# Optimization experiments

Measured on AMD Instinct MI355X. Metric: run time of the kernel, lower is better.

## Reference

```python
import jax, jax.numpy as jnp
import numpy as np

NEG_SLOPE = 0.01  # torch F.leaky_relu default

def _lrelu(x):
    return jax.nn.leaky_relu(x, NEG_SLOPE)

def setup_inputs() -> dict:
    key = jax.random.key(0)
    ks = jax.random.split(key, 24)
    B, N, E = 512, 20000, 640000
    n_enc_1, n_enc_2, n_z = 512, 256, 64
    n_dec_2, n_dec_1, hidden = 256, 512, 256
    p = lambda k, shp, fan: jax.random.normal(k, shp, jnp.float32) * (1.0 / np.sqrt(fan))
    return {
        "data": jax.random.normal(ks[0], (B, N), jnp.float32),
        "noise": jax.random.normal(ks[1], (B, N), jnp.float32),
        "edge_index": jax.random.randint(ks[2], (2, E), 0, N, jnp.int32),
        "w_gcn": jax.random.normal(ks[3], (), jnp.float32),
        "b_gcn": jax.random.normal(ks[4], (), jnp.float32) * 0.1,
        "enc1_w": p(ks[5], (N, n_enc_1), N), "enc1_b": p(ks[6], (n_enc_1,), N),
        "enc2_w": p(ks[7], (n_enc_1, n_enc_2), n_enc_1), "enc2_b": p(ks[8], (n_enc_2,), n_enc_1),
        "enc3_w": p(ks[9], (n_enc_2, n_z), n_enc_2), "enc3_b": p(ks[10], (n_z,), n_enc_2),
        "dec1_w": p(ks[11], (n_z, n_dec_2), n_z), "dec1_b": p(ks[12], (n_dec_2,), n_z),
        "dec2_w": p(ks[13], (n_dec_2, n_dec_1), n_dec_2), "dec2_b": p(ks[14], (n_dec_1,), n_dec_2),
        "dec3_w": p(ks[15], (n_dec_1, N), n_dec_1), "dec3_b": p(ks[16], (N,), n_dec_1),
        "disc1_w": p(ks[17], (n_z, hidden), n_z), "disc1_b": p(ks[18], (hidden,), n_z),
        "disc2_w": p(ks[19], (hidden, hidden), hidden), "disc2_b": p(ks[20], (hidden,), hidden),
        "disc3_w": p(ks[21], (hidden, 1), hidden), "disc3_b": p(ks[22], (1,), hidden),
    }

def _gcn_batched(x, edge_index, w_gcn, b_gcn):
    # x: [B, N] -> GCNConv(1,1, improved=True) applied per row, vectorized.
    B, N = x.shape
    src, dst = edge_index[0], edge_index[1]
    loop = jnp.arange(N, dtype=src.dtype)
    src_a = jnp.concatenate([src, loop])
    dst_a = jnp.concatenate([dst, loop])
    # improved=True: self-loop edge weight 2.0
    ew = jnp.concatenate([jnp.ones(src.shape[0], x.dtype), jnp.full((N,), 2.0, x.dtype)])
    deg = jax.ops.segment_sum(ew, dst_a, num_segments=N)
    dinv = jnp.where(deg > 0, jax.lax.rsqrt(deg), 0.0)
    norm = dinv[src_a] * ew * dinv[dst_a]  # [E+N]
    xl = x * w_gcn                         # lin (1x1 weight, no bias)
    msgs = xl[:, src_a] * norm[None, :]    # [B, E+N]
    agg = jnp.zeros_like(x).at[:, dst_a].add(msgs)
    return agg + b_gcn

def reference(data, noise, edge_index, w_gcn, b_gcn,
              enc1_w, enc1_b, enc2_w, enc2_b, enc3_w, enc3_b,
              dec1_w, dec1_b, dec2_w, dec2_b, dec3_w, dec3_b,
              disc1_w, disc1_b, disc2_w, disc2_b, disc3_w, disc3_b):
    x = data + noise * 0.1
    gcn_out = _lrelu(_gcn_batched(x, edge_index, w_gcn, b_gcn))  # [B, N]
    h1 = _lrelu(gcn_out @ enc1_w + enc1_b)
    h2 = _lrelu(h1 @ enc2_w + enc2_b)
    z = _lrelu(h2 @ enc3_w + enc3_b)
    d1 = _lrelu(z @ dec1_w + dec1_b)
    d2 = _lrelu(d1 @ dec2_w + dec2_b)
    dec_h3 = _lrelu(d2 @ dec3_w + dec3_b)
    g1 = _lrelu(z @ disc1_w + disc1_b)
    g2 = _lrelu(g1 @ disc2_w + disc2_b)
    d = jax.nn.sigmoid(g2 @ disc3_w + disc3_b)
    return (dec_h3, z, d)
```

## Files before the change

### kernel.cpp

```cpp
#include <hip/hip_runtime.h>
#include <hip/hip_bf16.h>


#define LRELU(v) ((v) > 0.f ? (v) : 0.01f * (v))

static constexpr int Bb = 512;
static constexpr int Nn = 20000;
static constexpr int Ee = 640000;
static constexpr int KPAD = 20480;
static constexpr int NPD = 20096;
static constexpr int RSU = 36;
static constexpr int RSW = 18;

typedef __attribute__((ext_vector_type(8))) short short8;
typedef __attribute__((ext_vector_type(4))) short short4v;
typedef __attribute__((ext_vector_type(4))) float f32x4;

__device__ __forceinline__ ushort f2bf(float f) {
  uint u = __builtin_bit_cast(uint, f);
  u = u + 0x7FFFu + ((u >> 16) & 1u);
  return (ushort)(u >> 16);
}
__device__ __forceinline__ float bfLo(uint u) {
  return __builtin_bit_cast(float, u << 16);
}
__device__ __forceinline__ float bfHi(uint u) {
  return __builtin_bit_cast(float, u & 0xffff0000u);
}

__global__ void transpose_xs_k(const float* __restrict__ a, const float* __restrict__ nz,
                               const float* __restrict__ dinv, ushort* __restrict__ xs) {
  __shared__ ushort tile[64][65];
  int c0 = blockIdx.x * 64;
  int p = blockIdx.y;
  int chunk = p >> 1;
  int sub = (p & 1) * 64;
  int rbase = p * 64;
  for (int i = threadIdx.x; i < 64 * 64; i += 256) {
    int rr = i >> 6, cc = i & 63;
    int r = rbase + rr, c = c0 + cc;
    ushort v = 0;
    if (c < Nn) {
      size_t idx = (size_t)r * Nn + c;
      v = f2bf(dinv[c] * (a[idx] + 0.1f * nz[idx]));
    }
    tile[rr][cc] = v;
  }
  __syncthreads();
  for (int i = threadIdx.x; i < 64 * 64; i += 256) {
    int cc = i >> 6, rr = i & 63;
    int c = c0 + cc;
    if (c < Nn) xs[(size_t)chunk * Nn * 128 + (size_t)c * 128 + sub + rr] = tile[rr][cc];
  }
}

__global__ void hist_check_k(const int* __restrict__ src, const int* __restrict__ dst, int E,
                             int* __restrict__ cnt, int* __restrict__ flag) {
  int i = blockIdx.x * 256 + threadIdx.x;
  if (i < E) {
    int s = src[i], d = dst[i];
    if ((unsigned)s >= (unsigned)Nn || (unsigned)d >= (unsigned)Nn) {
      atomicExch(flag, 1);
    } else {
      atomicAdd(&cnt[d], 1);
    }
  }
}

__global__ void offs_k(const int* __restrict__ cnt, int* __restrict__ offs,
                       int* __restrict__ cursor, float* __restrict__ dinv,
                       int* __restrict__ bump) {
  int i = blockIdx.x * 256 + threadIdx.x;
  int l = threadIdx.x & 63;
  int v = (i < Nn) ? cnt[i] : 0;
  int x = v;
#pragma unroll
  for (int d = 1; d < 64; d <<= 1) {
    int t = __shfl_up(x, d);
    if (l >= d) x += t;
  }
  int total = __shfl(x, 63);
  int base = 0;
  if (l == 0) base = atomicAdd(bump, total);
  base = __shfl(base, 0);
  int excl = base + x - v;
  if (i < Nn) {
    offs[i] = excl;
    cursor[i] = excl;
    dinv[i] = rsqrtf(2.0f + (float)v);
  }
}

__global__ void scatter_k(const int* __restrict__ src, const int* __restrict__ dst, int E,
                          int* __restrict__ cursor, uint* __restrict__ eOff) {
  int i = blockIdx.x * 256 + threadIdx.x;
  if (i < E) {
    int s = src[i], d = dst[i];
    if ((unsigned)s >= (unsigned)Nn || (unsigned)d >= (unsigned)Nn) return;
    int p = atomicAdd(&cursor[d], 1);
    eOff[p] = (uint)s * 256u;
  }
}

__global__ __launch_bounds__(256) void spmm_chunk_k(
    const ushort* __restrict__ xs, const uint* __restrict__ eOff, const int* __restrict__ offs,
    const int* __restrict__ cnt, const float* __restrict__ dinv, const float* __restrict__ wg,
    const float* __restrict__ bg, ushort* __restrict__ gcnT) {
  __shared__ uint sIdx[4][64];
  int bid = blockIdx.x;
  int chunk = bid & 3;
  int ngrp = bid >> 2;
  int wv = threadIdx.x >> 6, l = threadIdx.x & 63;
  int n = ngrp * 4 + wv;
  int o = offs[n], c = cnt[n];
  const char* base = (const char*)(xs + (size_t)chunk * Nn * 128) + l * 4;
  const uint* ep = eOff + o;
  uint su = *(const uint*)(base + (size_t)n * 256);
  float a00 = 2.0f * bfLo(su), a01 = 2.0f * bfHi(su);
  float a10 = 0.f, a11 = 0.f;

  for (int bi = 0; bi < c; bi += 64) {
    int rem = c - bi;
    if (rem > 64) rem = 64;
    sIdx[wv][l] = (l < rem) ? ep[bi + l] : 0u;
    int i = 0;
    for (; i + 8 <= rem; i += 8) {
      uint u[8];
#pragma unroll
      for (int j = 0; j < 8; ++j) u[j] = *(const uint*)(base + sIdx[wv][i + j]);
#pragma unroll
      for (int j = 0; j < 8; j += 2) {
        a00 += bfLo(u[j]);
        a01 += bfHi(u[j]);
        a10 += bfLo(u[j + 1]);
        a11 += bfHi(u[j + 1]);
      }
    }
    for (; i < rem; ++i) {
      uint u = *(const uint*)(base + sIdx[wv][i]);
      a00 += bfLo(u);
      a01 += bfHi(u);
    }
  }

  float wdn = wg[0] * dinv[n], bb = bg[0];
  float v0 = wdn * (a00 + a10) + bb;
  float v1 = wdn * (a01 + a11) + bb;
  v0 = LRELU(v0);
  v1 = LRELU(v1);
  uint pk = (uint)f2bf(v0) | ((uint)f2bf(v1) << 16);
  *(uint*)&gcnT[(size_t)chunk * KPAD * 128 + (size_t)n * 128 + 2 * l] = pk;
}

__global__ __launch_bounds__(256) void mfma_gemm4(const ushort* __restrict__ AT,
                                                  const float* __restrict__ B, int KB,
                                                  int iters, float* __restrict__ C) {
  __shared__ ushort As[128 * RSU];
  __shared__ ushort Bs[128 * RSU];
  int n0 = blockIdx.x * 128, m0 = blockIdx.y * 128;
  int k0 = blockIdx.z * iters * 32;
  int tid = threadIdx.x;
  int kp = tid >> 4;
  int cpr = tid & 15;
  int c8 = cpr * 8;
  int l = tid & 63, w = tid >> 6;
  int wr = w >> 1, wc = w & 1;
  int lrow = l & 15, lkg = l >> 4;
  const ushort* Ap = AT + (size_t)(m0 >> 7) * ((size_t)KPAD * 128);
  int bcol = n0 + c8;
  int kps = kp ^ (((cpr >> 1) & 3) << 2);
  f32x4 acc[4][4] = {};

  uint4 pa0, pa1;
  float4 pb00, pb01, pb10, pb11;

#define GLOAD(KG)                                                              \
  {                                                                            \
    int kq = (KG) + 2 * kp;                                                    \
    pa0 = *(const uint4*)&Ap[(size_t)kq * 128 + c8];                           \
    pa1 = *(const uint4*)&Ap[(size_t)(kq + 1) * 128 + c8];                     \
    pb00 = pb01 = pb10 = pb11 = float4{0.f, 0.f, 0.f, 0.f};                    \
    if (kq < KB) {                                                             \
      const float4* bp = (const float4*)(B + (size_t)kq * 512 + bcol);         \
      pb00 = bp[0];                                                            \
      pb01 = bp[1];                                                            \
    }                                                                          \
    if (kq + 1 < KB) {                                                         \
      const float4* bp = (const float4*)(B + (size_t)(kq + 1) * 512 + bcol);   \
      pb10 = bp[0];                                                            \
      pb11 = bp[1];                                                            \
    }                                                                          \
  }

  GLOAD(k0);

  for (int kt = 0; kt < iters; ++kt) {
    uint wa[8], wb[8];
    wa[0] = (pa0.x & 0xffffu) | (pa1.x << 16);
    wa[1] = (pa0.x >> 16) | (pa1.x & 0xffff0000u);
    wa[2] = (pa0.y & 0xffffu) | (pa1.y << 16);
    wa[3] = (pa0.y >> 16) | (pa1.y & 0xffff0000u);
    wa[4] = (pa0.z & 0xffffu) | (pa1.z << 16);
    wa[5] = (pa0.z >> 16) | (pa1.z & 0xffff0000u);
    wa[6] = (pa0.w & 0xffffu) | (pa1.w << 16);
    wa[7] = (pa0.w >> 16) | (pa1.w & 0xffff0000u);
    wb[0] = (uint)f2bf(pb00.x) | ((uint)f2bf(pb10.x) << 16);
    wb[1] = (uint)f2bf(pb00.y) | ((uint)f2bf(pb10.y) << 16);
    wb[2] = (uint)f2bf(pb00.z) | ((uint)f2bf(pb10.z) << 16);
    wb[3] = (uint)f2bf(pb00.w) | ((uint)f2bf(pb10.w) << 16);
    wb[4] = (uint)f2bf(pb01.x) | ((uint)f2bf(pb11.x) << 16);
    wb[5] = (uint)f2bf(pb01.y) | ((uint)f2bf(pb11.y) << 16);
    wb[6] = (uint)f2bf(pb01.z) | ((uint)f2bf(pb11.z) << 16);
    wb[7] = (uint)f2bf(pb01.w) | ((uint)f2bf(pb11.w) << 16);
    __syncthreads();
    {
      uint* aw = (uint*)As;
      uint* bw = (uint*)Bs;
#pragma unroll
      for (int j = 0; j < 8; ++j) {
        aw[(c8 + j) * RSW + kps] = wa[j];
        bw[(c8 + j) * RSW + kps] = wb[j];
      }
    }
    __syncthreads();
    if (kt + 1 < iters) GLOAD(k0 + (kt + 1) * 32);
    short8 a[4], b[4];
#pragma unroll
    for (int mi = 0; mi < 4; ++mi) {
      int m = wr * 64 + mi * 16 + lrow;
      int lk2 = lkg ^ ((wr * 4 + mi) & 3);
      const short4v* p = (const short4v*)&As[m * RSU + lk2 * 8];
      a[mi] = __builtin_shufflevector(p[0], p[1], 0, 1, 2, 3, 4, 5, 6, 7);
    }
#pragma unroll
    for (int nj = 0; nj < 4; ++nj) {
      int n = wc * 64 + nj * 16 + lrow;
      int lk2 = lkg ^ ((wc * 4 + nj) & 3);
      const short4v* p = (const short4v*)&Bs[n * RSU + lk2 * 8];
      b[nj] = __builtin_shufflevector(p[0], p[1], 0, 1, 2, 3, 4, 5, 6, 7);
    }
#pragma unroll
    for (int mi = 0; mi < 4; ++mi)
#pragma unroll
      for (int nj = 0; nj < 4; ++nj)
        acc[mi][nj] = __builtin_amdgcn_mfma_f32_16x16x32_bf16(a[mi], b[nj], acc[mi][nj], 0, 0, 0);
  }
#undef GLOAD

#pragma unroll
  for (int mi = 0; mi < 4; ++mi)
#pragma unroll
    for (int nj = 0; nj < 4; ++nj)
#pragma unroll
      for (int r = 0; r < 4; ++r) {
        int row = m0 + wr * 64 + mi * 16 + lkg * 4 + r;
        int col = n0 + wc * 64 + nj * 16 + lrow;
        atomicAdd(&C[(size_t)row * 512 + col], acc[mi][nj][r]);
      }
}

__global__ void conv_wf_k(const float* __restrict__ W, ushort* __restrict__ wf) {
  int n = blockIdx.x * 256 + threadIdx.x;
  int kb = blockIdx.y;
  if (n >= NPD) return;
  ushort v[8];
#pragma unroll
  for (int j = 0; j < 8; ++j)
    v[j] = (n < Nn) ? f2bf(W[(size_t)(8 * kb + j) * Nn + n]) : (ushort)0;
  uint4 pk;
  pk.x = (uint)v[0] | ((uint)v[1] << 16);
  pk.y = (uint)v[2] | ((uint)v[3] << 16);
  pk.z = (uint)v[4] | ((uint)v[5] << 16);
  pk.w = (uint)v[6] | ((uint)v[7] << 16);
  *(uint4*)&wf[((size_t)kb * NPD + n) * 8] = pk;
}

__global__ __launch_bounds__(256) void fmg_dec3_k(const ushort* __restrict__ d2f,
                                                  const ushort* __restrict__ wf,
                                                  const float* __restrict__ bias,
                                                  float* __restrict__ C) {
  int n0 = blockIdx.x * 128, m0 = blockIdx.y * 128;
  int l = threadIdx.x & 63, w = threadIdx.x >> 6;
  int wr = w >> 1, wc = w & 1;
  int lrow = l & 15, lkg = l >> 4;
  f32x4 acc[4][4] = {};

#pragma unroll 4
  for (int ks = 0; ks < 16; ++ks) {
    int kb = ks * 4 + lkg;
    short8 a[4], b[4];
#pragma unroll
    for (int mi = 0; mi < 4; ++mi) {
      int m = m0 + wr * 64 + mi * 16 + lrow;
      a[mi] = *(const short8*)&d2f[((size_t)kb * 512 + m) * 8];
    }
#pragma unroll
    for (int nj = 0; nj < 4; ++nj) {
      int n = n0 + wc * 64 + nj * 16 + lrow;
      b[nj] = *(const short8*)&wf[((size_t)kb * NPD + n) * 8];
    }
#pragma unroll
    for (int mi = 0; mi < 4; ++mi)
#pragma unroll
      for (int nj = 0; nj < 4; ++nj)
        acc[mi][nj] = __builtin_amdgcn_mfma_f32_16x16x32_bf16(a[mi], b[nj], acc[mi][nj], 0, 0, 0);
  }

#pragma unroll
  for (int mi = 0; mi < 4; ++mi)
#pragma unroll
    for (int nj = 0; nj < 4; ++nj)
#pragma unroll
      for (int r = 0; r < 4; ++r) {
        int row = m0 + wr * 64 + mi * 16 + lkg * 4 + r;
        int col = n0 + wc * 64 + nj * 16 + lrow;
        if (col < Nn) {
          float v = acc[mi][nj][r] + bias[col];
          C[(size_t)row * Nn + col] = LRELU(v);
        }
      }
}

__global__ __launch_bounds__(256) void tail2_k(
    const float* __restrict__ h1, const float* __restrict__ c1, const float* __restrict__ W2,
    const float* __restrict__ c2, const float* __restrict__ W3, const float* __restrict__ c3,
    const float* __restrict__ Wd1, const float* __restrict__ cd1, const float* __restrict__ Wd2,
    const float* __restrict__ cd2, const float* __restrict__ Wg1, const float* __restrict__ cg1,
    const float* __restrict__ Wg2, const float* __restrict__ cg2, const float* __restrict__ Wg3,
    const float* __restrict__ cg3, float* __restrict__ out_z, float* __restrict__ out_d,
    ushort* __restrict__ d2f) {
  __shared__ float s_h1[512];
  __shared__ float s_h2[256];
  __shared__ float s_z[64];
  __shared__ float s_d1[256];
  __shared__ float s_g1[256];
  __shared__ float s_g2[256];
  __shared__ float s_part[4][256];
  __shared__ float s_red[4];
  int rl = blockIdx.x;
  int t = threadIdx.x;
  int w = t >> 6, l = t & 63;

  {
    float r0 = h1[(size_t)rl * 512 + t] + c1[t];
    float r1 = h1[(size_t)rl * 512 + t + 256] + c1[t + 256];
    s_h1[t] = LRELU(r0);
    s_h1[t + 256] = LRELU(r1);
  }
  __syncthreads();

  {
    int c4 = l * 4;
    float a0 = 0.f, a1 = 0.f, a2 = 0.f, a3 = 0.f;
#pragma unroll 8
    for (int k = w * 128; k < w * 128 + 128; ++k) {
      float4 wv = *(const float4*)&W2[(size_t)k * 256 + c4];
      float x = s_h1[k];
      a0 += x * wv.x; a1 += x * wv.y; a2 += x * wv.z; a3 += x * wv.w;
    }
    float4 pv = {a0, a1, a2, a3};
    *(float4*)&s_part[w][c4] = pv;
  }
  __syncthreads();
  s_h2[t] = LRELU(s_part[0][t] + s_part[1][t] + s_part[2][t] + s_part[3][t] + c2[t]);
  __syncthreads();

  {
    int c = t >> 2, p = t & 3;
    float a = 0.f;
#pragma unroll 8
    for (int k = p * 64; k < p * 64 + 64; ++k) a += s_h2[k] * W3[(size_t)k * 64 + c];
    s_part[p][c] = a;
  }
  __syncthreads();
  if (t < 64) {
    float v = s_part[0][t] + s_part[1][t] + s_part[2][t] + s_part[3][t] + c3[t];
    v = LRELU(v);
    s_z[t] = v;
    out_z[(size_t)rl * 64 + t] = v;
  }
  __syncthreads();

  {
    float a = 0.f;
#pragma unroll
    for (int k = 0; k < 64; ++k) a += s_z[k] * Wd1[(size_t)k * 256 + t];
    s_d1[t] = LRELU(a + cd1[t]);
  }
  {
    float a = 0.f;
#pragma unroll
    for (int k = 0; k < 64; ++k) a += s_z[k] * Wg1[(size_t)k * 256 + t];
    s_g1[t] = LRELU(a + cg1[t]);
  }
  __syncthreads();

  {
    int g = t & 127, p = t >> 7;
    int c4 = g * 4;
    float a0 = 0.f, a1 = 0.f, a2 = 0.f, a3 = 0.f;
#pragma unroll 8
    for (int k = p * 128; k < p * 128 + 128; ++k) {
      float4 wv = *(const float4*)&Wd2[(size_t)k * 512 + c4];
      float x = s_d1[k];
      a0 += x * wv.x; a1 += x * wv.y; a2 += x * wv.z; a3 += x * wv.w;
    }
    float* sp = &s_part[0][0];
    float4 pv = {a0, a1, a2, a3};
    *(float4*)&sp[p * 512 + c4] = pv;
  }
  __syncthreads();
  {
    const float* sp = &s_part[0][0];
#pragma unroll
    for (int cc = 0; cc < 2; ++cc) {
      int c = t + cc * 256;
      float v = sp[c] + sp[512 + c] + cd2[c];
      v = LRELU(v);
      d2f[((size_t)(c >> 3) * 512 + rl) * 8 + (c & 7)] = f2bf(v);
    }
  }
  __syncthreads();

  {
    int c4 = l * 4;
    float a0 = 0.f, a1 = 0.f, a2 = 0.f, a3 = 0.f;
#pragma unroll 8
    for (int k = w * 64; k < w * 64 + 64; ++k) {
      float4 wv = *(const float4*)&Wg2[(size_t)k * 256 + c4];
      float x = s_g1[k];
      a0 += x * wv.x; a1 += x * wv.y; a2 += x * wv.z; a3 += x * wv.w;
    }
    float4 pv = {a0, a1, a2, a3};
    *(float4*)&s_part[w][c4] = pv;
  }
  __syncthreads();
  s_g2[t] = LRELU(s_part[0][t] + s_part[1][t] + s_part[2][t] + s_part[3][t] + cg2[t]);
  __syncthreads();

  {
    float p = s_g2[t] * Wg3[t];
#pragma unroll
    for (int o = 32; o > 0; o >>= 1) p += __shfl_down(p, o);
    if ((t & 63) == 0) s_red[t >> 6] = p;
    __syncthreads();
    if (t == 0) {
      float s = s_red[0] + s_red[1] + s_red[2] + s_red[3] + cg3[0];
      out_d[rl] = 1.f / (1.f + __expf(-s));
    }
  }
}

__global__ void sentinel_k(float* out, float val) { out[0] = val; }
__global__ void flag_sentinel_k(float* out, const int* flag) {
  if (*flag != 0) out[0] = 70000.0f;
}

extern "C" void kernel_launch(void* const* d_in, const int* in_sizes, int n_in,
                              void* d_out, int out_size, void* d_ws, size_t ws_size,
                              hipStream_t stream) {
  const float* data = (const float*)d_in[0];
  const float* noise = (const float*)d_in[1];
  const int* edge = (const int*)d_in[2];
  const int* esrc_in = edge;
  const int* edst_in = edge + Ee;
  const float* w_gcn = (const float*)d_in[3];
  const float* b_gcn = (const float*)d_in[4];
  const float* enc1_w = (const float*)d_in[5];
  const float* enc1_b = (const float*)d_in[6];
  const float* enc2_w = (const float*)d_in[7];
  const float* enc2_b = (const float*)d_in[8];
  const float* enc3_w = (const float*)d_in[9];
  const float* enc3_b = (const float*)d_in[10];
  const float* dec1_w = (const float*)d_in[11];
  const float* dec1_b = (const float*)d_in[12];
  const float* dec2_w = (const float*)d_in[13];
  const float* dec2_b = (const float*)d_in[14];
  const float* dec3_w = (const float*)d_in[15];
  const float* dec3_b = (const float*)d_in[16];
  const float* disc1_w = (const float*)d_in[17];
  const float* disc1_b = (const float*)d_in[18];
  const float* disc2_w = (const float*)d_in[19];
  const float* disc2_b = (const float*)d_in[20];
  const float* disc3_w = (const float*)d_in[21];
  const float* disc3_b = (const float*)d_in[22];

  char* w = (char*)d_ws;
  size_t o = 0;
  auto alloc = [&](size_t bytes) {
    size_t r = o;
    o = (o + bytes + 15) & ~(size_t)15;
    return r;
  };
  size_t r1 = alloc((size_t)64 * NPD * 8 * 2);
  ushort* xs = (ushort*)(w + r1);
  ushort* wf = (ushort*)(w + r1);
  ushort* gcnT = (ushort*)(w + alloc((size_t)4 * KPAD * 128 * 2));
  float* h1 = (float*)(w + alloc(512 * 512 * 4));
  ushort* d2f = (ushort*)(w + alloc((size_t)64 * 512 * 8 * 2));
  float* dinv = (float*)(w + alloc(Nn * 4));
  int* cnt = (int*)(w + alloc(Nn * 4));
  int* offs = (int*)(w + alloc(Nn * 4));
  int* cursor = (int*)(w + alloc(Nn * 4));
  uint* eOff = (uint*)(w + alloc(Ee * 4));
  int* flag = (int*)(w + alloc(16));

  float* outp = (float*)d_out;
  float* out_dec = outp;
  float* out_z = outp + (size_t)Bb * Nn;
  float* out_d = out_z + (size_t)Bb * 64;

  static const int expect_sizes[23] = {
      10240000, 10240000, 1280000, 1, 1,
      10240000, 512, 131072, 256, 16384, 64,
      16384, 256, 131072, 512, 10240000, 20000,
      16384, 256, 65536, 256, 256, 1};
  float host_sentinel = 0.f;
  if (n_in != 23) host_sentinel = 50000.f;
  else if (out_size != 10273280) host_sentinel = 80000.f;
  else if (ws_size < 46100000u) host_sentinel = 60000.f;
  else {
    for (int i = 0; i < 23; ++i)
      if (in_sizes[i] != expect_sizes[i]) { host_sentinel = 100000.f + 1000.f * i; break; }
  }

  hipMemsetAsync(cnt, 0, Nn * sizeof(int), stream);
  hipMemsetAsync(flag, 0, 2 * sizeof(int), stream);
  hist_check_k<<<(Ee + 255) / 256, 256, 0, stream>>>(esrc_in, edst_in, Ee, cnt, flag);
  offs_k<<<(Nn + 255) / 256, 256, 0, stream>>>(cnt, offs, cursor, dinv, flag + 1);
  scatter_k<<<(Ee + 255) / 256, 256, 0, stream>>>(esrc_in, edst_in, Ee, cursor, eOff);
  for (int c = 0; c < 4; ++c)
    hipMemsetAsync(gcnT + ((size_t)c * KPAD + Nn) * 128, 0, (size_t)(KPAD - Nn) * 128 * 2,
                   stream);

  {
    dim3 g((Nn + 63) / 64, 8);
    transpose_xs_k<<<g, 256, 0, stream>>>(data, noise, dinv, xs);
  }
  spmm_chunk_k<<<(Nn / 4) * 4, 256, 0, stream>>>(xs, eOff, offs, cnt, dinv, w_gcn, b_gcn, gcnT);
  hipMemsetAsync(h1, 0, 512 * 512 * 4, stream);
  {
    dim3 g(512 / 128, 512 / 128, 32);
    mfma_gemm4<<<g, 256, 0, stream>>>(gcnT, enc1_w, Nn, 20, h1);
  }
  tail2_k<<<Bb, 256, 0, stream>>>(h1, enc1_b, enc2_w, enc2_b, enc3_w, enc3_b, dec1_w, dec1_b,
                                  dec2_w, dec2_b, disc1_w, disc1_b, disc2_w, disc2_b, disc3_w,
                                  disc3_b, out_z, out_d, d2f);
  {
    dim3 g((NPD + 255) / 256, 64);
    conv_wf_k<<<g, 256, 0, stream>>>(dec3_w, wf);
  }
  {
    dim3 g(NPD / 128, 512 / 128);
    fmg_dec3_k<<<g, 256, 0, stream>>>(d2f, wf, dec3_b, out_dec);
  }

  flag_sentinel_k<<<1, 1, 0, stream>>>(out_dec, flag);
  if (host_sentinel != 0.f) sentinel_k<<<1, 1, 0, stream>>>(out_dec, host_sentinel);
}
```

Before: 288.2 us.

## Emit GCN output in MFMA fragment layout and pre-convert enc1 weights for LDS-free GEMM

```diff
diff --git a/kernel.cpp b/kernel.cpp
--- a/kernel.cpp
+++ b/kernel.cpp
@@ -7,13 +7,10 @@
 static constexpr int Bb = 512;
 static constexpr int Nn = 20000;
 static constexpr int Ee = 640000;
-static constexpr int KPAD = 20480;
+static constexpr int KBn = 2500;
 static constexpr int NPD = 20096;
-static constexpr int RSU = 36;
-static constexpr int RSW = 18;
 
 typedef __attribute__((ext_vector_type(8))) short short8;
-typedef __attribute__((ext_vector_type(4))) short short4v;
 typedef __attribute__((ext_vector_type(4))) float f32x4;
 
 __device__ __forceinline__ ushort f2bf(float f) {
@@ -102,142 +99,104 @@
   }
 }
 
-__global__ __launch_bounds__(256) void spmm_chunk_k(
+__global__ __launch_bounds__(256) void spmm_fm_k(
     const ushort* __restrict__ xs, const uint* __restrict__ eOff, const int* __restrict__ offs,
     const int* __restrict__ cnt, const float* __restrict__ dinv, const float* __restrict__ wg,
-    const float* __restrict__ bg, ushort* __restrict__ gcnT) {
+    const float* __restrict__ bg, ushort* __restrict__ gfm) {
   __shared__ uint sIdx[4][64];
+  __shared__ ushort sOut[128][8];
   int bid = blockIdx.x;
   int chunk = bid & 3;
-  int ngrp = bid >> 2;
+  int grp = bid >> 2;
   int wv = threadIdx.x >> 6, l = threadIdx.x & 63;
-  int n = ngrp * 4 + wv;
-  int o = offs[n], c = cnt[n];
   const char* base = (const char*)(xs + (size_t)chunk * Nn * 128) + l * 4;
-  const uint* ep = eOff + o;
-  uint su = *(const uint*)(base + (size_t)n * 256);
-  float a00 = 2.0f * bfLo(su), a01 = 2.0f * bfHi(su);
-  float a10 = 0.f, a11 = 0.f;
-
-  for (int bi = 0; bi < c; bi += 64) {
-    int rem = c - bi;
-    if (rem > 64) rem = 64;
-    sIdx[wv][l] = (l < rem) ? ep[bi + l] : 0u;
-    int i = 0;
-    for (; i + 8 <= rem; i += 8) {
-      uint u[8];
-#pragma unroll
-      for (int j = 0; j < 8; ++j) u[j] = *(const uint*)(base + sIdx[wv][i + j]);
-#pragma unroll
-      for (int j = 0; j < 8; j += 2) {
-        a00 += bfLo(u[j]);
-        a01 += bfHi(u[j]);
-        a10 += bfLo(u[j + 1]);
-        a11 += bfHi(u[j + 1]);
+  float wgv = wg[0], bb = bg[0];
+
+#pragma unroll
+  for (int sub = 0; sub < 2; ++sub) {
+    int n = grp * 8 + wv * 2 + sub;
+    int o = offs[n], c = cnt[n];
+    const uint* ep = eOff + o;
+    uint su = *(const uint*)(base + (size_t)n * 256);
+    float a00 = 2.0f * bfLo(su), a01 = 2.0f * bfHi(su);
+    float a10 = 0.f, a11 = 0.f;
+
+    for (int bi = 0; bi < c; bi += 64) {
+      int rem = c - bi;
+      if (rem > 64) rem = 64;
+      sIdx[wv][l] = (l < rem) ? ep[bi + l] : 0u;
+      int i = 0;
+      for (; i + 8 <= rem; i += 8) {
+        uint u[8];
+#pragma unroll
+        for (int j = 0; j < 8; ++j) u[j] = *(const uint*)(base + sIdx[wv][i + j]);
+#pragma unroll
+        for (int j = 0; j < 8; j += 2) {
+          a00 += bfLo(u[j]);
+          a01 += bfHi(u[j]);
+          a10 += bfLo(u[j + 1]);
+          a11 += bfHi(u[j + 1]);
+        }
       }
-    }
-    for (; i < rem; ++i) {
-      uint u = *(const uint*)(base + sIdx[wv][i]);
-      a00 += bfLo(u);
-      a01 += bfHi(u);
-    }
-  }
-
-  float wdn = wg[0] * dinv[n], bb = bg[0];
-  float v0 = wdn * (a00 + a10) + bb;
-  float v1 = wdn * (a01 + a11) + bb;
-  v0 = LRELU(v0);
-  v1 = LRELU(v1);
-  uint pk = (uint)f2bf(v0) | ((uint)f2bf(v1) << 16);
-  *(uint*)&gcnT[(size_t)chunk * KPAD * 128 + (size_t)n * 128 + 2 * l] = pk;
-}
-
-__global__ __launch_bounds__(256) void mfma_gemm4(const ushort* __restrict__ AT,
-                                                  const float* __restrict__ B, int KB,
-                                                  int iters, float* __restrict__ C) {
-  __shared__ ushort As[128 * RSU];
-  __shared__ ushort Bs[128 * RSU];
+      for (; i < rem; ++i) {
+        uint u = *(const uint*)(base + sIdx[wv][i]);
+        a00 += bfLo(u);
+        a01 += bfHi(u);
+      }
+    }
+
+    float wdn = wgv * dinv[n];
+    float v0 = wdn * (a00 + a10) + bb;
+    float v1 = wdn * (a01 + a11) + bb;
+    v0 = LRELU(v0);
+    v1 = LRELU(v1);
+    int j = wv * 2 + sub;
+    sOut[2 * l][j] = f2bf(v0);
+    sOut[2 * l + 1][j] = f2bf(v1);
+  }
+  __syncthreads();
+  int row = threadIdx.x >> 1, half = threadIdx.x & 1;
+  uint2 v = *(const uint2*)&sOut[row][half * 4];
+  int m = chunk * 128 + row;
+  *(uint2*)&gfm[((size_t)grp * 512 + m) * 8 + half * 4] = v;
+}
+
+__global__ void conv_we_k(const float* __restrict__ W, ushort* __restrict__ wef) {
+  int n = blockIdx.x * 256 + threadIdx.x;
+  int kb = blockIdx.y;
+  ushort v[8];
+#pragma unroll
+  for (int j = 0; j < 8; ++j) v[j] = f2bf(W[(size_t)(8 * kb + j) * 512 + n]);
+  uint4 pk;
+  pk.x = (uint)v[0] | ((uint)v[1] << 16);
+  pk.y = (uint)v[2] | ((uint)v[3] << 16);
+  pk.z = (uint)v[4] | ((uint)v[5] << 16);
+  pk.w = (uint)v[6] | ((uint)v[7] << 16);
+  *(uint4*)&wef[((size_t)kb * 512 + n) * 8] = pk;
+}
+
+__global__ __launch_bounds__(256) void fmg_enc1_k(const ushort* __restrict__ gfm,
+                                                  const ushort* __restrict__ wef,
+                                                  float* __restrict__ C) {
   int n0 = blockIdx.x * 128, m0 = blockIdx.y * 128;
-  int k0 = blockIdx.z * iters * 32;
-  int tid = threadIdx.x;
-  int kp = tid >> 4;
-  int cpr = tid & 15;
-  int c8 = cpr * 8;
-  int l = tid & 63, w = tid >> 6;
+  int l = threadIdx.x & 63, w = threadIdx.x >> 6;
   int wr = w >> 1, wc = w & 1;
   int lrow = l & 15, lkg = l >> 4;
-  const ushort* Ap = AT + (size_t)(m0 >> 7) * ((size_t)KPAD * 128);
-  int bcol = n0 + c8;
-  int kps = kp ^ (((cpr >> 1) & 3) << 2);
   f32x4 acc[4][4] = {};
-
-  uint4 pa0, pa1;
-  float4 pb00, pb01, pb10, pb11;
-
-#define GLOAD(KG)                                                              \
-  {                                                                            \
-    int kq = (KG) + 2 * kp;                                                    \
-    pa0 = *(const uint4*)&Ap[(size_t)kq * 128 + c8];                           \
-    pa1 = *(const uint4*)&Ap[(size_t)(kq + 1) * 128 + c8];                     \
-    pb00 = pb01 = pb10 = pb11 = float4{0.f, 0.f, 0.f, 0.f};                    \
-    if (kq < KB) {                                                             \
-      const float4* bp = (const float4*)(B + (size_t)kq * 512 + bcol);         \
-      pb00 = bp[0];                                                            \
-      pb01 = bp[1];                                                            \
-    }                                                                          \
-    if (kq + 1 < KB) {                                                         \
-      const float4* bp = (const float4*)(B + (size_t)(kq + 1) * 512 + bcol);   \
-      pb10 = bp[0];                                                            \
-      pb11 = bp[1];                                                            \
-    }                                                                          \
-  }
-
-  GLOAD(k0);
-
-  for (int kt = 0; kt < iters; ++kt) {
-    uint wa[8], wb[8];
-    wa[0] = (pa0.x & 0xffffu) | (pa1.x << 16);
-    wa[1] = (pa0.x >> 16) | (pa1.x & 0xffff0000u);
-    wa[2] = (pa0.y & 0xffffu) | (pa1.y << 16);
-    wa[3] = (pa0.y >> 16) | (pa1.y & 0xffff0000u);
-    wa[4] = (pa0.z & 0xffffu) | (pa1.z << 16);
-    wa[5] = (pa0.z >> 16) | (pa1.z & 0xffff0000u);
-    wa[6] = (pa0.w & 0xffffu) | (pa1.w << 16);
-    wa[7] = (pa0.w >> 16) | (pa1.w & 0xffff0000u);
-    wb[0] = (uint)f2bf(pb00.x) | ((uint)f2bf(pb10.x) << 16);
-    wb[1] = (uint)f2bf(pb00.y) | ((uint)f2bf(pb10.y) << 16);
-    wb[2] = (uint)f2bf(pb00.z) | ((uint)f2bf(pb10.z) << 16);
-    wb[3] = (uint)f2bf(pb00.w) | ((uint)f2bf(pb10.w) << 16);
-    wb[4] = (uint)f2bf(pb01.x) | ((uint)f2bf(pb11.x) << 16);
-    wb[5] = (uint)f2bf(pb01.y) | ((uint)f2bf(pb11.y) << 16);
-    wb[6] = (uint)f2bf(pb01.z) | ((uint)f2bf(pb11.z) << 16);
-    wb[7] = (uint)f2bf(pb01.w) | ((uint)f2bf(pb11.w) << 16);
-    __syncthreads();
-    {
-      uint* aw = (uint*)As;
-      uint* bw = (uint*)Bs;
-#pragma unroll
-      for (int j = 0; j < 8; ++j) {
-        aw[(c8 + j) * RSW + kps] = wa[j];
-        bw[(c8 + j) * RSW + kps] = wb[j];
-      }
-    }
-    __syncthreads();
-    if (kt + 1 < iters) GLOAD(k0 + (kt + 1) * 32);
+  int ksBeg = blockIdx.z * 25, ksEnd = ksBeg + 25;
+
+  for (int ks = ksBeg; ks < ksEnd; ++ks) {
+    int kb = ks * 4 + lkg;
     short8 a[4], b[4];
 #pragma unroll
     for (int mi = 0; mi < 4; ++mi) {
-      int m = wr * 64 + mi * 16 + lrow;
-      int lk2 = lkg ^ ((wr * 4 + mi) & 3);
-      const short4v* p = (const short4v*)&As[m * RSU + lk2 * 8];
-      a[mi] = __builtin_shufflevector(p[0], p[1], 0, 1, 2, 3, 4, 5, 6, 7);
+      int m = m0 + wr * 64 + mi * 16 + lrow;
+      a[mi] = *(const short8*)&gfm[((size_t)kb * 512 + m) * 8];
     }
 #pragma unroll
     for (int nj = 0; nj < 4; ++nj) {
-      int n = wc * 64 + nj * 16 + lrow;
-      int lk2 = lkg ^ ((wc * 4 + nj) & 3);
-      const short4v* p = (const short4v*)&Bs[n * RSU + lk2 * 8];
-      b[nj] = __builtin_shufflevector(p[0], p[1], 0, 1, 2, 3, 4, 5, 6, 7);
+      int n = n0 + wc * 64 + nj * 16 + lrow;
+      b[nj] = *(const short8*)&wef[((size_t)kb * 512 + n) * 8];
     }
 #pragma unroll
     for (int mi = 0; mi < 4; ++mi)
@@ -245,7 +204,6 @@
       for (int nj = 0; nj < 4; ++nj)
         acc[mi][nj] = __builtin_amdgcn_mfma_f32_16x16x32_bf16(a[mi], b[nj], acc[mi][nj], 0, 0, 0);
   }
-#undef GLOAD
 
 #pragma unroll
   for (int mi = 0; mi < 4; ++mi)
@@ -494,8 +452,9 @@
   };
   size_t r1 = alloc((size_t)64 * NPD * 8 * 2);
   ushort* xs = (ushort*)(w + r1);
+  ushort* wef = (ushort*)(w + r1);
   ushort* wf = (ushort*)(w + r1);
-  ushort* gcnT = (ushort*)(w + alloc((size_t)4 * KPAD * 128 * 2));
+  ushort* gfm = (ushort*)(w + alloc((size_t)KBn * 512 * 8 * 2));
   float* h1 = (float*)(w + alloc(512 * 512 * 4));
   ushort* d2f = (ushort*)(w + alloc((size_t)64 * 512 * 8 * 2));
   float* dinv = (float*)(w + alloc(Nn * 4));
@@ -529,19 +488,20 @@
   hist_check_k<<<(Ee + 255) / 256, 256, 0, stream>>>(esrc_in, edst_in, Ee, cnt, flag);
   offs_k<<<(Nn + 255) / 256, 256, 0, stream>>>(cnt, offs, cursor, dinv, flag + 1);
   scatter_k<<<(Ee + 255) / 256, 256, 0, stream>>>(esrc_in, edst_in, Ee, cursor, eOff);
-  for (int c = 0; c < 4; ++c)
-    hipMemsetAsync(gcnT + ((size_t)c * KPAD + Nn) * 128, 0, (size_t)(KPAD - Nn) * 128 * 2,
-                   stream);
 
   {
     dim3 g((Nn + 63) / 64, 8);
     transpose_xs_k<<<g, 256, 0, stream>>>(data, noise, dinv, xs);
   }
-  spmm_chunk_k<<<(Nn / 4) * 4, 256, 0, stream>>>(xs, eOff, offs, cnt, dinv, w_gcn, b_gcn, gcnT);
+  spmm_fm_k<<<(Nn / 8) * 4, 256, 0, stream>>>(xs, eOff, offs, cnt, dinv, w_gcn, b_gcn, gfm);
+  {
+    dim3 g(2, KBn);
+    conv_we_k<<<g, 256, 0, stream>>>(enc1_w, wef);
+  }
   hipMemsetAsync(h1, 0, 512 * 512 * 4, stream);
   {
-    dim3 g(512 / 128, 512 / 128, 32);
-    mfma_gemm4<<<g, 256, 0, stream>>>(gcnT, enc1_w, Nn, 20, h1);
+    dim3 g(512 / 128, 512 / 128, 25);
+    fmg_enc1_k<<<g, 256, 0, stream>>>(gfm, wef, h1);
   }
   tail2_k<<<Bb, 256, 0, stream>>>(h1, enc1_b, enc2_w, enc2_b, enc3_w, enc3_b, dec1_w, dec1_b,
                                   dec2_w, dec2_b, disc1_w, disc1_b, disc2_w, disc2_b, disc3_w,
```

Measured after the change: 288.9 us. Within noise of the previous version (+0.2%).
